# Kernel optimization log

Measured on AMD Instinct MI355X. Metric: run time of the kernel, lower is better.

Reference implementation:

```python
import jax, jax.numpy as jnp
import numpy as np

N, C = 65536, 1000

def setup_inputs() -> dict:
    key = jax.random.key(0)
    k1, k2 = jax.random.split(key)
    inp = jax.random.normal(k1, (N, C), dtype=jnp.float32)
    tgt = jax.random.randint(k2, (N,), 0, C, dtype=jnp.int64)
    return {"input": inp, "target": tgt}

def reference(input, target):
    # sign mask: +1 at the target class, -1 elsewhere (replaces the scatter loop)
    one_hot = jnp.arange(input.shape[1])[None, :] == target[:, None]  # [N, C] bool
    m = jnp.where(one_hot, input, -input)
    # piecewise huber-hinge: if m >= -1 -> max(0, 1-m)^2 else -4*m
    hinge = jnp.maximum(0.0, 1.0 - m)
    loss = jnp.where(m >= -1.0, hinge * hinge, -4.0 * m)
    return jnp.sum(loss) / target.shape[0]
```

## Files before the change

kernel.cpp:

```cpp
#include <hip/hip_runtime.h>


typedef float f4 __attribute__((ext_vector_type(4)));

constexpr int N_ROWS = 65536;
constexpr int N_COLS = 1000;
constexpr int F4_PER_ROW = N_COLS / 4;
constexpr int TOTAL_F4 = N_ROWS * F4_PER_ROW;

constexpr int GRID = 2000;
constexpr int BLOCK = 256;
constexpr int STRIDE_F4 = GRID * BLOCK;
constexpr int STRIDE_ROWS = STRIDE_F4 / F4_PER_ROW;
constexpr int ITERS = TOTAL_F4 / STRIDE_F4;
constexpr int BATCH = 8;

__global__ __launch_bounds__(BLOCK) void mhl_kernel(const f4* __restrict__ in,
                                                    const int* __restrict__ tgt,
                                                    float* __restrict__ out) {
    int idx = blockIdx.x * BLOCK + threadIdx.x;

    int row = idx / F4_PER_ROW;
    int c0 = (idx - row * F4_PER_ROW) * 4;
    int p = idx;

    float acc = 0.0f;

#pragma unroll 1
    for (int it = 0; it < ITERS / BATCH; ++it) {
        f4 v[BATCH];
        int t[BATCH];
#pragma unroll
        for (int j = 0; j < BATCH; ++j) {
            v[j] = __builtin_nontemporal_load(&in[p + j * STRIDE_F4]);
            t[j] = tgt[row + j * STRIDE_ROWS];
        }
#pragma unroll
        for (int j = 0; j < BATCH; ++j) {
#pragma unroll
            for (int e = 0; e < 4; ++e) {
                float x = v[j][e];
                float m = (c0 + e == t[j]) ? x : -x;
                float h = fmaxf(0.0f, 1.0f - m);
                float l = (m >= -1.0f) ? h * h : -4.0f * m;
                acc += l;
            }
        }
        p += BATCH * STRIDE_F4;
        row += BATCH * STRIDE_ROWS;
    }

#pragma unroll
    for (int off = 32; off > 0; off >>= 1)
        acc += __shfl_down(acc, off, 64);

    __shared__ float wsum[BLOCK / 64];
    int wid = threadIdx.x >> 6;
    int lane = threadIdx.x & 63;
    if (lane == 0) wsum[wid] = acc;
    __syncthreads();

    if (threadIdx.x == 0) {
        float s = wsum[0] + wsum[1] + wsum[2] + wsum[3];
        atomicAdd(out, s * (1.0f / (float)N_ROWS));
    }
}

extern "C" void kernel_launch(void* const* d_in, const int* in_sizes, int n_in,
                              void* d_out, int out_size, void* d_ws, size_t ws_size,
                              hipStream_t stream) {
    const f4* in = (const f4*)d_in[0];
    const int* tgt = (const int*)d_in[1];
    float* out = (float*)d_out;

    (void)hipMemsetAsync(out, 0, sizeof(float), stream);

    mhl_kernel<<<GRID, BLOCK, 0, stream>>>(in, tgt, out);
}
```

Measured before the change: 57.81 us.

## Compute loss as uniform negative-margin sum plus per-row target correction blocks

Rewrites the loss algebraically: every element is treated as a non-target (m = -x) using a branchless clamp-based form, and a separate set of 64 blocks adds the per-row correction f(target) - f(non-target) by gathering one element per row. This removes the per-element target comparison and the target loads from the streaming loop. The streaming loads also drop the nontemporal hint. The cost is an extra scattered gather pass over 65536 elements and floating-point summation order changes.

```diff
diff --git a/kernel.cpp b/kernel.cpp
--- a/kernel.cpp
+++ b/kernel.cpp
@@ -8,46 +8,53 @@
 constexpr int F4_PER_ROW = N_COLS / 4;
 constexpr int TOTAL_F4 = N_ROWS * F4_PER_ROW;
 
-constexpr int GRID = 2000;
 constexpr int BLOCK = 256;
-constexpr int STRIDE_F4 = GRID * BLOCK;
-constexpr int STRIDE_ROWS = STRIDE_F4 / F4_PER_ROW;
+constexpr int MAIN_GRID = 2000;
+constexpr int CORR_GRID = 64;
+constexpr int STRIDE_F4 = MAIN_GRID * BLOCK;
 constexpr int ITERS = TOTAL_F4 / STRIDE_F4;
 constexpr int BATCH = 8;
 
+__device__ __forceinline__ float huber_f(float h) {
+    float hc = fmaxf(fminf(h, 2.0f), 0.0f);
+    return hc * fmaf(h, 2.0f, -hc);
+}
+
 __global__ __launch_bounds__(BLOCK) void mhl_kernel(const f4* __restrict__ in,
+                                                    const float* __restrict__ in_f,
                                                     const int* __restrict__ tgt,
                                                     float* __restrict__ out) {
-    int idx = blockIdx.x * BLOCK + threadIdx.x;
-
-    int row = idx / F4_PER_ROW;
-    int c0 = (idx - row * F4_PER_ROW) * 4;
-    int p = idx;
-
     float acc = 0.0f;
 
+    if (blockIdx.x < CORR_GRID) {
+        int tid = blockIdx.x * BLOCK + threadIdx.x;
+#pragma unroll
+        for (int k = 0; k < 4; ++k) {
+            int r = tid + k * (CORR_GRID * BLOCK);
+            int t = tgt[r];
+            float x = in_f[r * N_COLS + t];
+            acc += huber_f(1.0f - x) - huber_f(1.0f + x);
+        }
+    } else {
+        int idx = (blockIdx.x - CORR_GRID) * BLOCK + threadIdx.x;
+        int p = idx;
 #pragma unroll 1
-    for (int it = 0; it < ITERS / BATCH; ++it) {
-        f4 v[BATCH];
-        int t[BATCH];
+        for (int it = 0; it < ITERS / BATCH; ++it) {
+            f4 v[BATCH];
 #pragma unroll
-        for (int j = 0; j < BATCH; ++j) {
-            v[j] = __builtin_nontemporal_load(&in[p + j * STRIDE_F4]);
-            t[j] = tgt[row + j * STRIDE_ROWS];
+            for (int j = 0; j < BATCH; ++j)
+                v[j] = in[p + j * STRIDE_F4];
+#pragma unroll
+            for (int j = 0; j < BATCH; ++j) {
+#pragma unroll
+                for (int e = 0; e < 4; ++e) {
+                    float h = 1.0f + v[j][e];
+                    float hc = fmaxf(fminf(h, 2.0f), 0.0f);
+                    acc = fmaf(hc, fmaf(h, 2.0f, -hc), acc);
+                }
+            }
+            p += BATCH * STRIDE_F4;
         }
-#pragma unroll
-        for (int j = 0; j < BATCH; ++j) {
-#pragma unroll
-            for (int e = 0; e < 4; ++e) {
-                float x = v[j][e];
-                float m = (c0 + e == t[j]) ? x : -x;
-                float h = fmaxf(0.0f, 1.0f - m);
-                float l = (m >= -1.0f) ? h * h : -4.0f * m;
-                acc += l;
-            }
-        }
-        p += BATCH * STRIDE_F4;
-        row += BATCH * STRIDE_ROWS;
     }
 
 #pragma unroll
@@ -70,10 +77,11 @@
                               void* d_out, int out_size, void* d_ws, size_t ws_size,
                               hipStream_t stream) {
     const f4* in = (const f4*)d_in[0];
+    const float* in_f = (const float*)d_in[0];
     const int* tgt = (const int*)d_in[1];
     float* out = (float*)d_out;
 
     (void)hipMemsetAsync(out, 0, sizeof(float), stream);
 
-    mhl_kernel<<<GRID, BLOCK, 0, stream>>>(in, tgt, out);
+    mhl_kernel<<<MAIN_GRID + CORR_GRID, BLOCK, 0, stream>>>(in, in_f, tgt, out);
 }
```

Measured after the change: 58.66 us. Within noise of the previous version (+1.5%).
